# Kernel optimization log

Hardware: AMD Instinct MI355X
Metric: run time of the kernel (lower is better)

## Reference

```python
import jax, jax.numpy as jnp
import numpy as np

# Model config (matches init_kwargs)
DAG_DEPTH = 16
HIDDEN = 2048
B, T = 4, 4096
N = DAG_DEPTH                 # total_nodes
INIT_SLOTS = DAG_DEPTH // 2   # initial slots
INTER = DAG_DEPTH // 2        # intermediate slots / scan steps
LOG_CLAMP = 23.026
SIGN_TEMP = 1e-4


def _xavier(k, shape):
    fan_out, fan_in = shape
    lim = np.sqrt(6.0 / (fan_in + fan_out)).astype(np.float32)
    return jax.random.uniform(k, shape, jnp.float32, -lim, lim)


def setup_inputs() -> dict:
    key = jax.random.key(0)
    k0, k1, k2, k3 = jax.random.split(key, 4)
    return {
        "hidden": jax.random.normal(k0, (B, T, HIDDEN), jnp.float32),
        "W_init": _xavier(k1, (2 * N, HIDDEN)),
        "b_init": jnp.zeros((2 * N,), jnp.float32),
        "W_op": _xavier(k2, (INTER * N, HIDDEN)),
        "b_op": jnp.zeros((INTER * N,), jnp.float32),
        "W_gate": _xavier(k3, (INTER, HIDDEN)),
        "b_gate": jnp.zeros((INTER,), jnp.float32),
    }


def reference(hidden, W_init, b_init, W_op, b_op, W_gate, b_gate):
    Bb, Tt, H = hidden.shape
    # --- plan predictor ---
    init_raw = jnp.einsum('bth,oh->bto', hidden, W_init) + b_init        # (B,T,2N)
    V_mag = jnp.abs(init_raw[..., :N])                                   # (B,T,N)
    V_sign = jnp.tanh(init_raw[..., N:])                                 # (B,T,N)
    O = (jnp.einsum('bth,oh->bto', hidden, W_op) + b_op).reshape(Bb, Tt, INTER, N)
    G = jax.nn.sigmoid(jnp.einsum('bth,oh->bto', hidden, W_gate) + b_gate)  # (B,T,INTER)

    # --- sequential DAG execution (fixed INTER steps, vectorized over B,T) ---
    # NOTE: torch casts to float64 (float32 on mps); here we compute in float32,
    # identical math modulo precision (jax x64 is disabled by default).
    pos = jnp.arange(N)
    for step in range(INTER):
        valid = INIT_SLOTS + step
        mask = (pos < valid).astype(hidden.dtype)                        # causal mask over nodes
        O_s = O[:, :, step, :] * mask                                    # (B,T,N)
        G_s = G[:, :, step:step + 1]                                     # (B,T,1)
        signed = V_sign * V_mag
        log_mag = jnp.log(jnp.clip(V_mag, 1e-12))
        mixed = log_mag * (1.0 - G_s) + signed * G_s
        R = jnp.sum(O_s * mixed, axis=-1, keepdims=True)                 # (B,T,1)
        lin_sign = jnp.tanh(R / SIGN_TEMP)
        sign_prod = jnp.prod(V_sign * (jnp.abs(O_s) + 1.0), axis=-1, keepdims=True)
        log_sign = jnp.tanh(sign_prod / SIGN_TEMP)
        Vs_new = G_s * lin_sign + (1.0 - G_s) * log_sign
        Vm_new = G_s * jnp.abs(R) + (1.0 - G_s) * jnp.exp(jnp.clip(R, None, LOG_CLAMP))
        idx = INIT_SLOTS + step
        V_mag = V_mag.at[:, :, idx].set(Vm_new[..., 0])
        V_sign = V_sign.at[:, :, idx].set(Vs_new[..., 0])

    return V_sign[:, :, -1] * V_mag[:, :, -1]                            # (B,T)
```

## Files before the change

kernel.cpp:

```cpp
#include <hip/hip_runtime.h>
#include <math.h>

#define HID    2048
#define NROW   16384
#define NCOL   168
#define BM     32
#define KSTEPS 64
#define NELEM  2112
#define CPD    172
#define NSLOT  16
#define NSTEP  8

typedef short short8 __attribute__((ext_vector_type(8)));
typedef float f32x4  __attribute__((ext_vector_type(4)));
typedef unsigned int u32x4 __attribute__((ext_vector_type(4)));

static __device__ __forceinline__ unsigned pack_hi(unsigned u0, unsigned u1) {
  return __builtin_amdgcn_perm(u1, u0, 0x07060302u);
}

struct Planes { u32x4 p1, p2, p3; };
static __device__ __forceinline__ Planes split8(const float* x) {
  Planes P;
  #pragma unroll
  for (int q = 0; q < 4; ++q) {
    float x0 = x[2*q], x1 = x[2*q+1];
    unsigned u0 = __float_as_uint(x0), u1 = __float_as_uint(x1);
    P.p1[q] = pack_hi(u0, u1);
    float r0 = x0 - __uint_as_float(u0 & 0xFFFF0000u);
    float r1 = x1 - __uint_as_float(u1 & 0xFFFF0000u);
    unsigned v0 = __float_as_uint(r0), v1 = __float_as_uint(r1);
    P.p2[q] = pack_hi(v0, v1);
    float s0 = r0 - __uint_as_float(v0 & 0xFFFF0000u);
    float s1 = r1 - __uint_as_float(v1 & 0xFFFF0000u);
    P.p3[q] = pack_hi(__float_as_uint(s0), __float_as_uint(s1));
  }
  return P;
}

static __device__ __forceinline__ void loadA8(const float* p, float* x) {
  f32x4 a = *(const f32x4*)p;
  f32x4 b = *(const f32x4*)(p + 4);
  x[0]=a[0]; x[1]=a[1]; x[2]=a[2]; x[3]=a[3];
  x[4]=b[0]; x[5]=b[1]; x[6]=b[2]; x[7]=b[3];
}

static __device__ __forceinline__ f32x4 mf(short8 a, short8 b, f32x4 c) {
  return __builtin_amdgcn_mfma_f32_16x16x32_bf16(a, b, c, 0, 0, 0);
}

__global__ void prep_b(const float* __restrict__ Wi, const float* __restrict__ Wo,
                       const float* __restrict__ Wg, u32x4* __restrict__ wsB) {
  int bid  = blockIdx.x;
  int kidx = bid / 11;
  int nt   = bid - kidx * 11;
  int l    = threadIdx.x;
  int col  = nt * 16 + (l & 15);
  int k0   = kidx * 32 + (l >> 4) * 8;

  float x[8];
  if (col < NCOL) {
    const float* wr = (col < 32)  ? (Wi + (size_t)col * HID)
                    : (col < 160) ? (Wo + (size_t)(col - 32) * HID)
                                  : (Wg + (size_t)(col - 160) * HID);
    loadA8(wr + k0, x);
  } else {
    #pragma unroll
    for (int i = 0; i < 8; ++i) x[i] = 0.f;
  }
  Planes P = split8(x);
  size_t base = (size_t)kidx * NELEM + (nt * 3) * 64 + l;
  wsB[base]       = P.p1;
  wsB[base + 64]  = P.p2;
  wsB[base + 128] = P.p3;
}

__global__ __launch_bounds__(256, 3)
void dag_main(const float* __restrict__ hidden, const u32x4* __restrict__ wsB,
              const float* __restrict__ b_init, const float* __restrict__ b_op,
              const float* __restrict__ b_gate, float* __restrict__ out)
{
  __shared__ float sC[BM][CPD];

  const int tid = threadIdx.x;
  const int l   = tid & 63;
  const int w   = tid >> 6;
  const int row0 = blockIdx.x * BM;
  const int r   = l & 15;
  const int kg  = l >> 4;

  const float* ap0 = hidden + (size_t)(row0 + r) * HID + kg * 8;
  const float* ap1 = ap0 + (size_t)16 * HID;

  const u32x4* bbase = wsB + (size_t)(w * 9) * 64 + l;

  f32x4 acc[2][3];
  const f32x4 zf = {0.f, 0.f, 0.f, 0.f};
  #pragma unroll
  for (int mt = 0; mt < 2; ++mt)
    #pragma unroll
    for (int j = 0; j < 3; ++j) acc[mt][j] = zf;

  float xc0[8], xc1[8], xn0[8], xn1[8];
  u32x4 bc[9], bn[9];

#define LOADB(dst_, t_) do {                                   \
    const u32x4* s_ = bbase + (size_t)NELEM * (t_);            \
    dst_[0] = s_[0 * 64]; dst_[1] = s_[1 * 64];                \
    dst_[2] = s_[2 * 64]; dst_[3] = s_[3 * 64];                \
    dst_[4] = s_[4 * 64]; dst_[5] = s_[5 * 64];                \
    if (w != 3) {                                              \
      dst_[6] = s_[6 * 64]; dst_[7] = s_[7 * 64];              \
      dst_[8] = s_[8 * 64];                                    \
    }                                                          \
  } while (0)

#define STEP(bcur_, bnxt_, x0c_, x1c_, x0n_, x1n_, t_) do {                 \
    Planes PA0 = split8(x0c_);                                              \
    Planes PA1 = split8(x1c_);                                              \
    short8 a0p1 = __builtin_bit_cast(short8, PA0.p1);                       \
    short8 a0p2 = __builtin_bit_cast(short8, PA0.p2);                       \
    short8 a0p3 = __builtin_bit_cast(short8, PA0.p3);                       \
    short8 a1p1 = __builtin_bit_cast(short8, PA1.p1);                       \
    short8 a1p2 = __builtin_bit_cast(short8, PA1.p2);                       \
    short8 a1p3 = __builtin_bit_cast(short8, PA1.p3);                       \
    if ((t_) + 1 < KSTEPS) {                                                \
      loadA8(ap0 + ((t_) + 1) * 32, x0n_);                                  \
      loadA8(ap1 + ((t_) + 1) * 32, x1n_);                                  \
      LOADB(bnxt_, (t_) + 1);                                               \
    }                                                                       \
           \
    __builtin_amdgcn_sched_barrier(0);                                      \
    __builtin_amdgcn_s_setprio(1);                                          \
    _Pragma("unroll")                                                       \
    for (int j = 0; j < 3; ++j) {                                           \
      if (w == 3 && j == 2) continue;                                       \
      short8 b1 = __builtin_bit_cast(short8, bcur_[j * 3 + 0]);             \
      short8 b2 = __builtin_bit_cast(short8, bcur_[j * 3 + 1]);             \
      short8 b3 = __builtin_bit_cast(short8, bcur_[j * 3 + 2]);             \
      {                                                                     \
        f32x4 c = acc[0][j];                                                \
        c = mf(a0p1, b1, c); c = mf(a0p1, b2, c); c = mf(a0p2, b1, c);      \
        c = mf(a0p1, b3, c); c = mf(a0p2, b2, c); c = mf(a0p3, b1, c);      \
        acc[0][j] = c;                                                      \
      }                                                                     \
      {                                                                     \
        f32x4 c = acc[1][j];                                                \
        c = mf(a1p1, b1, c); c = mf(a1p1, b2, c); c = mf(a1p2, b1, c);      \
        c = mf(a1p1, b3, c); c = mf(a1p2, b2, c); c = mf(a1p3, b1, c);      \
        acc[1][j] = c;                                                      \
      }                                                                     \
    }                                                                       \
    __builtin_amdgcn_s_setprio(0);                                          \
  } while (0)

  loadA8(ap0, xc0);
  loadA8(ap1, xc1);
  LOADB(bc, 0);

  for (int t = 0; t < KSTEPS; t += 2) {
    STEP(bc, bn, xc0, xc1, xn0, xn1, t);
    STEP(bn, bc, xn0, xn1, xc0, xc1, t + 1);
  }
#undef STEP
#undef LOADB

  #pragma unroll
  for (int mt = 0; mt < 2; ++mt) {
    #pragma unroll
    for (int j = 0; j < 3; ++j) {
      int col = w * 48 + j * 16 + r;
      if (col < NCOL) {
        int row = mt * 16 + kg * 4;
        sC[row + 0][col] = acc[mt][j][0];
        sC[row + 1][col] = acc[mt][j][1];
        sC[row + 2][col] = acc[mt][j][2];
        sC[row + 3][col] = acc[mt][j][3];
      }
    }
  }
  __syncthreads();

  if (tid < BM) {
    const int rr = tid;
    float Vm[NSLOT], Vs[NSLOT];
    #pragma unroll
    for (int i = 0; i < NSLOT; ++i) {
      float mv = sC[rr][i]      + b_init[i];
      float sv = sC[rr][16 + i] + b_init[16 + i];
      Vm[i] = fabsf(mv);
      Vs[i] = tanhf(sv);
    }
    float G[NSTEP];
    #pragma unroll
    for (int s = 0; s < NSTEP; ++s) {
      float gr = sC[rr][160 + s] + b_gate[s];
      G[s] = 1.0f / (1.0f + expf(-gr));
    }
    #pragma unroll
    for (int s = 0; s < NSTEP; ++s) {
      const float g = G[s];
      float R = 0.f, sp = 1.f;
      #pragma unroll
      for (int i = 0; i < NSLOT; ++i) {
        float Osi = (i < 8 + s) ? (sC[rr][32 + s * 16 + i] + b_op[s * 16 + i]) : 0.f;
        float sgn   = Vs[i] * Vm[i];
        float logm  = logf(fmaxf(Vm[i], 1e-12f));
        float mixed = logm * (1.f - g) + sgn * g;
        R  += Osi * mixed;
        sp *= Vs[i] * (fabsf(Osi) + 1.f);
      }
      float lin_sign = tanhf(R  / 1e-4f);
      float log_sign = tanhf(sp / 1e-4f);
      float vs_new = g * lin_sign + (1.f - g) * log_sign;
      float vm_new = g * fabsf(R) + (1.f - g) * expf(fminf(R, 23.026f));
      Vm[8 + s] = vm_new;
      Vs[8 + s] = vs_new;
    }
    out[row0 + rr] = Vs[NSLOT - 1] * Vm[NSLOT - 1];
  }
}

extern "C" void kernel_launch(void* const* d_in, const int* in_sizes, int n_in,
                              void* d_out, int out_size, void* d_ws, size_t ws_size,
                              hipStream_t stream) {
  (void)in_sizes; (void)n_in; (void)out_size; (void)ws_size;
  const float* hidden = (const float*)d_in[0];
  const float* W_init = (const float*)d_in[1];
  const float* b_init = (const float*)d_in[2];
  const float* W_op   = (const float*)d_in[3];
  const float* b_op   = (const float*)d_in[4];
  const float* W_gate = (const float*)d_in[5];
  const float* b_gate = (const float*)d_in[6];
  float* out = (float*)d_out;
  u32x4* wsB = (u32x4*)d_ws;

  prep_b<<<dim3(704), dim3(64), 0, stream>>>(W_init, W_op, W_gate, wsB);
  dag_main<<<dim3(NROW / BM), dim3(256), 0, stream>>>(hidden, wsB, b_init, b_op,
                                                      b_gate, out);
}
```

Measured before the change: 116.2 us.

## Stage B operand tiles into LDS via async global_load_lds double buffering

Pre-split weight planes are no longer loaded into registers. Each wave now streams its B tiles straight into a two-deep LDS ring with global_load_lds, and A rows are prefetched two k-steps ahead. Explicit vmcnt/lgkmcnt waits replace the compiler's scheduling, with the aim of hiding global latency and freeing VGPRs. The larger LDS footprint lowers launch bounds from 3 to 2 blocks per CU. The hand-counted vmcnt(13) wait also relies on an exact count of in-flight loads per wave, which is fragile.

```diff
diff --git a/kernel.cpp b/kernel.cpp
--- a/kernel.cpp
+++ b/kernel.cpp
@@ -7,6 +7,7 @@
 #define BM     32
 #define KSTEPS 64
 #define NELEM  2112
+#define BUFB   33792
 #define CPD    172
 #define NSLOT  16
 #define NSTEP  8
@@ -14,6 +15,16 @@
 typedef short short8 __attribute__((ext_vector_type(8)));
 typedef float f32x4  __attribute__((ext_vector_type(4)));
 typedef unsigned int u32x4 __attribute__((ext_vector_type(4)));
+
+static __device__ __forceinline__ void wait_vm13() {
+  asm volatile("s_waitcnt vmcnt(13)" ::: "memory");
+}
+static __device__ __forceinline__ void wait_vm0() {
+  asm volatile("s_waitcnt vmcnt(0)" ::: "memory");
+}
+static __device__ __forceinline__ void wait_lgkm0() {
+  asm volatile("s_waitcnt lgkmcnt(0)" ::: "memory");
+}
 
 static __device__ __forceinline__ unsigned pack_hi(unsigned u0, unsigned u1) {
   return __builtin_amdgcn_perm(u1, u0, 0x07060302u);
@@ -49,6 +60,12 @@
   return __builtin_amdgcn_mfma_f32_16x16x32_bf16(a, b, c, 0, 0, 0);
 }
 
+static __device__ __forceinline__ void gld_lds16(const void* g, void* l) {
+  __builtin_amdgcn_global_load_lds(
+      (const __attribute__((address_space(1))) unsigned int*)g,
+      (__attribute__((address_space(3))) unsigned int*)l, 16, 0, 0);
+}
+
 __global__ void prep_b(const float* __restrict__ Wi, const float* __restrict__ Wo,
                        const float* __restrict__ Wg, u32x4* __restrict__ wsB) {
   int bid  = blockIdx.x;
@@ -75,12 +92,12 @@
   wsB[base + 128] = P.p3;
 }
 
-__global__ __launch_bounds__(256, 3)
+__global__ __launch_bounds__(256, 2)
 void dag_main(const float* __restrict__ hidden, const u32x4* __restrict__ wsB,
               const float* __restrict__ b_init, const float* __restrict__ b_op,
               const float* __restrict__ b_gate, float* __restrict__ out)
 {
-  __shared__ float sC[BM][CPD];
+  __shared__ __align__(16) char smem[2 * BUFB];
 
   const int tid = threadIdx.x;
   const int l   = tid & 63;
@@ -92,7 +109,16 @@
   const float* ap0 = hidden + (size_t)(row0 + r) * HID + kg * 8;
   const float* ap1 = ap0 + (size_t)16 * HID;
 
-  const u32x4* bbase = wsB + (size_t)(w * 9) * 64 + l;
+  const u32x4* gsrc[9];
+  char* ldst[9];
+  #pragma unroll
+  for (int i = 0; i < 9; ++i) {
+    int ii = (w == 3 && i >= 6) ? i - 6 : i;
+    int c  = 9 * w + ii;
+    gsrc[i] = wsB + (size_t)c * 64 + l;
+    ldst[i] = smem + c * 1024;
+  }
+  const char* brd0 = smem + (size_t)(9 * w) * 1024 + (size_t)l * 16;
 
   f32x4 acc[2][3];
   const f32x4 zf = {0.f, 0.f, 0.f, 0.f};
@@ -101,43 +127,44 @@
     #pragma unroll
     for (int j = 0; j < 3; ++j) acc[mt][j] = zf;
 
-  float xc0[8], xc1[8], xn0[8], xn1[8];
-  u32x4 bc[9], bn[9];
-
-#define LOADB(dst_, t_) do {                                   \
-    const u32x4* s_ = bbase + (size_t)NELEM * (t_);            \
-    dst_[0] = s_[0 * 64]; dst_[1] = s_[1 * 64];                \
-    dst_[2] = s_[2 * 64]; dst_[3] = s_[3 * 64];                \
-    dst_[4] = s_[4 * 64]; dst_[5] = s_[5 * 64];                \
-    if (w != 3) {                                              \
-      dst_[6] = s_[6 * 64]; dst_[7] = s_[7 * 64];              \
-      dst_[8] = s_[8 * 64];                                    \
-    }                                                          \
+  float xa0[8], xa1[8], xb0[8], xb1[8];
+
+#define STAGE(t_, sel_) do {                                                \
+    _Pragma("unroll")                                                       \
+    for (int i = 0; i < 9; ++i)                                             \
+      gld_lds16(gsrc[i] + (size_t)NELEM * (t_), ldst[i] + (sel_) * BUFB);   \
   } while (0)
 
-#define STEP(bcur_, bnxt_, x0c_, x1c_, x0n_, x1n_, t_) do {                 \
-    Planes PA0 = split8(x0c_);                                              \
-    Planes PA1 = split8(x1c_);                                              \
+#define BODY(t_, p_, xc0_, xc1_, ISSUE_, LAST_) do {                        \
+    if (LAST_) wait_vm0(); else wait_vm13();                                \
+    __builtin_amdgcn_sched_barrier(0);                                      \
+    const char* bb = brd0 + (p_) * BUFB;                                    \
+    short8 bf[9];                                                           \
+    _Pragma("unroll")                                                       \
+    for (int i = 0; i < 9; ++i)                                             \
+      if (w != 3 || i < 6) bf[i] = *(const short8*)(bb + i * 1024);         \
+    wait_lgkm0();     \
+    __builtin_amdgcn_sched_barrier(0);                                      \
+    if (ISSUE_) STAGE((t_) + 2, (p_));                                      \
+    Planes PA0 = split8(xc0_);                                              \
+    Planes PA1 = split8(xc1_);                                              \
+    if (ISSUE_) {                                                           \
+      loadA8(ap0 + ((t_) + 2) * 32, xc0_);                                  \
+      loadA8(ap1 + ((t_) + 2) * 32, xc1_);                                  \
+    }                                                                       \
     short8 a0p1 = __builtin_bit_cast(short8, PA0.p1);                       \
     short8 a0p2 = __builtin_bit_cast(short8, PA0.p2);                       \
     short8 a0p3 = __builtin_bit_cast(short8, PA0.p3);                       \
     short8 a1p1 = __builtin_bit_cast(short8, PA1.p1);                       \
     short8 a1p2 = __builtin_bit_cast(short8, PA1.p2);                       \
     short8 a1p3 = __builtin_bit_cast(short8, PA1.p3);                       \
-    if ((t_) + 1 < KSTEPS) {                                                \
-      loadA8(ap0 + ((t_) + 1) * 32, x0n_);                                  \
-      loadA8(ap1 + ((t_) + 1) * 32, x1n_);                                  \
-      LOADB(bnxt_, (t_) + 1);                                               \
-    }                                                                       \
-           \
-    __builtin_amdgcn_sched_barrier(0);                                      \
     __builtin_amdgcn_s_setprio(1);                                          \
     _Pragma("unroll")                                                       \
     for (int j = 0; j < 3; ++j) {                                           \
       if (w == 3 && j == 2) continue;                                       \
-      short8 b1 = __builtin_bit_cast(short8, bcur_[j * 3 + 0]);             \
-      short8 b2 = __builtin_bit_cast(short8, bcur_[j * 3 + 1]);             \
-      short8 b3 = __builtin_bit_cast(short8, bcur_[j * 3 + 2]);             \
+      short8 b1 = bf[j * 3 + 0];                                            \
+      short8 b2 = bf[j * 3 + 1];                                            \
+      short8 b3 = bf[j * 3 + 2];                                            \
       {                                                                     \
         f32x4 c = acc[0][j];                                                \
         c = mf(a0p1, b1, c); c = mf(a0p1, b2, c); c = mf(a0p2, b1, c);      \
@@ -154,17 +181,24 @@
     __builtin_amdgcn_s_setprio(0);                                          \
   } while (0)
 
-  loadA8(ap0, xc0);
-  loadA8(ap1, xc1);
-  LOADB(bc, 0);
-
-  for (int t = 0; t < KSTEPS; t += 2) {
-    STEP(bc, bn, xc0, xc1, xn0, xn1, t);
-    STEP(bn, bc, xn0, xn1, xc0, xc1, t + 1);
-  }
-#undef STEP
-#undef LOADB
-
+  STAGE(0, 0);
+  loadA8(ap0,      xa0);
+  loadA8(ap1,      xa1);
+  STAGE(1, 1);
+  loadA8(ap0 + 32, xb0);
+  loadA8(ap1 + 32, xb1);
+
+  for (int t = 0; t < 62; t += 2) {
+    BODY(t,     0, xa0, xa1, true, false);
+    BODY(t + 1, 1, xb0, xb1, true, false);
+  }
+  BODY(62, 0, xa0, xa1, false, false);
+  BODY(63, 1, xb0, xb1, false, true);
+#undef BODY
+#undef STAGE
+
+  __syncthreads();
+  float (*sC)[CPD] = (float(*)[CPD])smem;
   #pragma unroll
   for (int mt = 0; mt < 2; ++mt) {
     #pragma unroll
```

Result: no change. 115.3 us (-0.8%).
